# Kernel tuning notes

Hardware: AMD Instinct MI355X
Metric: run time of the kernel (lower is better)

Reference implementation:

```python
import jax, jax.numpy as jnp
import numpy as np

D_MODEL = 512
N_HEADS = 8
D_K = D_MODEL // N_HEADS


def setup_inputs() -> dict:
    key = jax.random.key(0)
    ks = jax.random.split(key, 12)
    B, L = 2, 512
    s = 1.0 / np.sqrt(D_MODEL)
    sk = 1.0 / np.sqrt(D_K)
    return {
        "query": jax.random.normal(ks[0], (B, L, D_MODEL), jnp.float32),
        "key": jax.random.normal(ks[1], (B, L, D_MODEL), jnp.float32),
        "value": jax.random.normal(ks[2], (B, L, D_MODEL), jnp.float32),
        "Wq": jax.random.normal(ks[3], (D_MODEL, D_MODEL), jnp.float32) * s,
        "bq": jnp.zeros((D_MODEL,), jnp.float32),
        "Wk": jax.random.normal(ks[4], (D_MODEL, D_MODEL), jnp.float32) * s,
        "bk": jnp.zeros((D_MODEL,), jnp.float32),
        "Wv": jax.random.normal(ks[5], (D_MODEL, D_MODEL), jnp.float32) * s,
        "bv": jnp.zeros((D_MODEL,), jnp.float32),
        "Wo": jax.random.normal(ks[6], (D_MODEL, D_MODEL), jnp.float32) * s,
        "bo": jnp.zeros((D_MODEL,), jnp.float32),
        "Aq": jax.random.normal(ks[7], (D_K, D_K), jnp.float32) * sk,  # inner W_q (no bias)
        "Ak": jax.random.normal(ks[8], (D_K, D_K), jnp.float32) * sk,  # inner W_k (no bias)
        "av": jax.random.normal(ks[9], (D_K,), jnp.float32) * sk,      # inner v (d_k -> 1)
    }


def _split_heads(x):
    B, L, _ = x.shape
    return x.reshape(B, L, N_HEADS, D_K).transpose(0, 2, 1, 3)  # [B,H,L,dk]


def reference(query, key, value, Wq, bq, Wk, bk, Wv, bv, Wo, bo, Aq, Ak, av):
    # outer projections (torch Linear: x @ W.T + b)
    Q = _split_heads(query @ Wq.T + bq)   # [B,H,Lq,dk]
    K = _split_heads(key @ Wk.T + bk)     # [B,H,Lk,dk]
    V = _split_heads(value @ Wv.T + bv)   # [B,H,Lk,dk]
    # inner additive attention: e_ij = v^T tanh(Aq q_i + Ak k_j)
    qp = Q @ Aq.T                          # [B,H,Lq,dk]
    kp = K @ Ak.T                          # [B,H,Lk,dk]
    energy = jnp.tanh(qp[:, :, :, None, :] + kp[:, :, None, :, :])  # [B,H,Lq,Lk,dk]
    scores = jnp.einsum('bhqkd,d->bhqk', energy, av)
    attn = jax.nn.softmax(scores, axis=-1)  # dropout disabled (eval)
    out = jnp.einsum('bhqk,bhkd->bhqd', attn, V)  # [B,H,Lq,dk]
    B, _, Lq, _ = out.shape
    out = out.transpose(0, 2, 1, 3).reshape(B, Lq, D_MODEL)
    return out @ Wo.T + bo
```

## Files before the change

kernel.cpp:

```cpp
#include <hip/hip_runtime.h>

#define LOG2E 1.4426950408889634f

typedef __bf16 bf16x8 __attribute__((ext_vector_type(8)));
typedef float f32x4 __attribute__((ext_vector_type(4)));
typedef float f32x2 __attribute__((ext_vector_type(2)));
typedef unsigned short u16x8 __attribute__((ext_vector_type(8)));

__device__ __forceinline__ unsigned short bfb(__bf16 b){
  union { __bf16 b; unsigned short u; } z; z.b = b; return z.u;
}


__global__ __launch_bounds__(256) void prep_all(
    const float* __restrict__ Wq, const float* __restrict__ Aq,
    const float* __restrict__ Wk, const float* __restrict__ Ak,
    const float* __restrict__ bq, const float* __restrict__ bk,
    const float* __restrict__ av,
    const float* __restrict__ Wv, const float* __restrict__ Wo,
    const float* __restrict__ Qin, const float* __restrict__ Kin,
    const float* __restrict__ Vin,
    unsigned short* __restrict__ W2qp, unsigned short* __restrict__ W2kp,
    unsigned short* __restrict__ Wvp,  unsigned short* __restrict__ Wop,
    unsigned short* __restrict__ qhi, unsigned short* __restrict__ qlo,
    unsigned short* __restrict__ khi, unsigned short* __restrict__ klo,
    unsigned short* __restrict__ vhi, unsigned short* __restrict__ vlo,
    float* __restrict__ b2q, float* __restrict__ b2k, float* __restrict__ av2g,
    float* __restrict__ zbase){
  if (blockIdx.x >= 513){
    if (blockIdx.y){
      int x = blockIdx.x - 513;
      if (x < 260){
        float* z = zbase + (size_t)(x * 256 + threadIdx.x) * 8;
        f32x4 zz = {0.f, 0.f, 0.f, 0.f};
        *(f32x4*)z = zz;
        *(f32x4*)(z + 4) = zz;
      }
      return;
    }
    int j = blockIdx.x - 513;
    const float* src; unsigned short *dh, *dl;
    if (j < 256){ src = Qin; dh = qhi; dl = qlo; }
    else if (j < 512){ src = Kin; dh = khi; dl = klo; j -= 256; }
    else { src = Vin; dh = vhi; dl = vlo; j -= 512; }
    int base = (j * 256 + threadIdx.x) * 8;
    f32x4 v0 = *(const f32x4*)(src + base);
    f32x4 v1 = *(const f32x4*)(src + base + 4);
    u16x8 hh, ll;
    #pragma unroll
    for (int t = 0; t < 8; t++){
      float f = (t < 4) ? v0[t] : v1[t - 4];
      __bf16 hb = (__bf16)f;
      hh[t] = bfb(hb);
      ll[t] = bfb((__bf16)(f - (float)hb));
    }
    *(u16x8*)(dh + base) = hh;
    *(u16x8*)(dl + base) = ll;
    return;
  }
  if (blockIdx.x >= 256){
    if (blockIdx.x == 512){
      if (blockIdx.y == 0){
        #pragma unroll
        for (int rep = 0; rep < 2; rep++){
          int n = rep * 256 + threadIdx.x;
          int h = n >> 6, e = n & 63;
          float aq = 0.f, ak = 0.f;
          for (int c = 0; c < 64; c++){
            aq += Aq[e*64 + c] * bq[h*64 + c];
            ak += Ak[e*64 + c] * bk[h*64 + c];
          }
          b2q[n] = aq * (2.f * LOG2E);
          b2k[n] = ak * (2.f * LOG2E);
        }
      } else {
        if (threadIdx.x < 64) av2g[threadIdx.x] = -2.f * LOG2E * av[threadIdx.x];
      }
      return;
    }
    const float* src = blockIdx.y ? Wo : Wv;
    unsigned short* dst = blockIdx.y ? Wop : Wvp;
    int base = ((blockIdx.x - 256) * 256 + threadIdx.x) * 4;
    int n = base >> 9, k0 = base & 511;
    float4 v = *(const float4*)(src + base);
    ushort4 h, l;
    float f; __bf16 hb;
    f = v.x; hb = (__bf16)f; h.x = bfb(hb); l.x = bfb((__bf16)(f - (float)hb));
    f = v.y; hb = (__bf16)f; h.y = bfb(hb); l.y = bfb((__bf16)(f - (float)hb));
    f = v.z; hb = (__bf16)f; h.z = bfb(hb); l.z = bfb((__bf16)(f - (float)hb));
    f = v.w; hb = (__bf16)f; h.w = bfb(hb); l.w = bfb((__bf16)(f - (float)hb));
    int nt = n >> 4, ln = n & 15;
    int ks = k0 >> 5, q = (k0 & 31) >> 3, j0 = k0 & 7;
    size_t off = (size_t)((nt*16 + ks) * 2) * 512 + (q*16 + ln) * 8 + j0;
    *(ushort4*)(dst + off)       = h;
    *(ushort4*)(dst + off + 512) = l;
    return;
  }
  const float* W  = blockIdx.y ? Wk : Wq;
  const float* Am = blockIdx.y ? Ak : Aq;
  unsigned short* dst = blockIdx.y ? W2kp : W2qp;
  int idx = blockIdx.x * 256 + threadIdx.x;
  int n = idx >> 7;
  int k0 = (idx & 127) * 4;
  int h = n >> 6, e = n & 63;
  float4 acc = {0.f, 0.f, 0.f, 0.f};
  #pragma unroll 8
  for (int c = 0; c < 64; c++){
    float am = Am[e*64 + c];
    float4 wv = *(const float4*)(W + (size_t)(h*64 + c)*512 + k0);
    acc.x += am * wv.x;
    acc.y += am * wv.y;
    acc.z += am * wv.z;
    acc.w += am * wv.w;
  }
  int nt = n >> 4, ln = n & 15;
  int ks = k0 >> 5, q = (k0 & 31) >> 3, j0 = k0 & 7;
  size_t off = (size_t)((nt*16 + ks) * 2) * 512 + (q*16 + ln) * 8 + j0;
  ushort4 hh, ll;
  float f; __bf16 hb;
  f = acc.x * (2.f * LOG2E); hb = (__bf16)f; hh.x = bfb(hb); ll.x = bfb((__bf16)(f - (float)hb));
  f = acc.y * (2.f * LOG2E); hb = (__bf16)f; hh.y = bfb(hb); ll.y = bfb((__bf16)(f - (float)hb));
  f = acc.z * (2.f * LOG2E); hb = (__bf16)f; hh.z = bfb(hb); ll.z = bfb((__bf16)(f - (float)hb));
  f = acc.w * (2.f * LOG2E); hb = (__bf16)f; hh.w = bfb(hb); ll.w = bfb((__bf16)(f - (float)hb));
  *(ushort4*)(dst + off)       = hh;
  *(ushort4*)(dst + off + 512) = ll;
}

struct GemmBatch {
  const unsigned short* Ahi;
  const unsigned short* Alo;
  const unsigned short* Bp;
  const float* bias;
  float* Cf;
  unsigned short* Chi;
  unsigned short* Clo;
  int transposed;
  int expout;
  int dual;
};
struct GemmArgs { GemmBatch g[3]; };

__global__ __launch_bounds__(256) void gemm_nk(GemmArgs ga){
  GemmBatch gb = ga.g[blockIdx.z];
  __shared__ unsigned short AhiS[64 * 40];
  __shared__ unsigned short AloS[64 * 40];
  const int tid = threadIdx.x, lane = tid & 63, w = tid >> 6;
  const int l15 = lane & 15, quad = lane >> 4;
  const int m0  = blockIdx.x * 32;
  const int nt0 = blockIdx.y * 4;
  const int wr = w >> 1, wc = w & 1;
  f32x4 ac0 = {0.f,0.f,0.f,0.f}, ac1 = ac0;

  const int srow = tid >> 3;
  const int scol = (tid & 7) * 8;
  const unsigned short* srcH = gb.Ahi + (size_t)(m0 + srow) * 512 + scol;
  const unsigned short* srcL = gb.Alo + (size_t)(m0 + srow) * 512 + scol;
  unsigned short* dstH = &AhiS[srow * 72 + scol];
  unsigned short* dstL = &AloS[srow * 72 + scol];
  u16x8 ph = *(const u16x8*)srcH;
  u16x8 pl = *(const u16x8*)srcL;

  const int arow = (wr * 16 + l15) * 72;

  for (int kc = 0; kc < 8; kc++){
    __syncthreads();
    *(u16x8*)dstH = ph;
    *(u16x8*)dstL = pl;
    if (kc < 7){
      ph = *(const u16x8*)(srcH + (kc + 1) * 64);
      pl = *(const u16x8*)(srcL + (kc + 1) * 64);
    }
    __syncthreads();
    #pragma unroll
    for (int s = 0; s < 2; s++){
      int ks = kc * 2 + s;
      bf16x8 ah = *(const bf16x8*)&AhiS[arow + s*32 + quad*8];
      bf16x8 al = *(const bf16x8*)&AloS[arow + s*32 + quad*8];
      #pragma unroll
      for (int t = 0; t < 2; t++){
        int nt = nt0 + wc*2 + t;
        const unsigned short* bp = gb.Bp + (size_t)((nt*16 + ks) * 2) * 512 + lane*8;
        bf16x8 bh = *(const bf16x8*)bp;
        bf16x8 bl = *(const bf16x8*)(bp + 512);
        f32x4& ac = t ? ac1 : ac0;
        ac = __builtin_amdgcn_mfma_f32_16x16x32_bf16(ah, bh, ac, 0, 0, 0);
        ac = __builtin_amdgcn_mfma_f32_16x16x32_bf16(al, bh, ac, 0, 0, 0);
        ac = __builtin_amdgcn_mfma_f32_16x16x32_bf16(ah, bl, ac, 0, 0, 0);
      }
    }
  }

  if (gb.dual){
    __syncthreads();
    #pragma unroll
    for (int t = 0; t < 2; t++){
      f32x4 v = t ? ac1 : ac0;
      int nl = wc*32 + t*16 + l15;
      float bs = gb.bias[nt0*16 + nl];
      #pragma unroll
      for (int r = 0; r < 4; r++){
        float val = v[r] + bs;
        int ml = wr*16 + quad*4 + r;
        __bf16 hb = (__bf16)val;
        AhiS[nl*40 + ml] = bfb(hb);
        AloS[nl*40 + ml] = bfb((__bf16)(val - (float)hb));
      }
    }
    __syncthreads();
    int nl = tid >> 2, mq = (tid & 3) * 8;
    int hh2 = (nt0 * 16) >> 6;
    int b2 = m0 >> 9;
    size_t o = (size_t)((b2*8 + hh2)*64 + ((nt0*16 + nl) & 63)) * 512 + (m0 & 511) + mq;
    *(u16x8*)(gb.Chi + o) = *(const u16x8*)&AhiS[nl*40 + mq];
    *(u16x8*)(gb.Clo + o) = *(const u16x8*)&AloS[nl*40 + mq];
    return;
  }

  const int mrow = m0 + wr * 16 + quad * 4;
  #pragma unroll
  for (int t = 0; t < 2; t++){
    f32x4 v = t ? ac1 : ac0;
    int n = nt0*16 + wc*32 + t*16 + l15;
    float bs = gb.bias[n];
    #pragma unroll
    for (int r = 0; r < 4; r++){
      float val = v[r] + bs;
      if (gb.expout) val = __builtin_amdgcn_exp2f(val);
      int m2 = mrow + r;
      if (gb.transposed){
        gb.Cf[(size_t)(((m2 >> 9) * 8 + (n >> 6)) * 512 + (m2 & 511)) * 64 + (n & 63)] = val;
      } else {
        gb.Cf[(size_t)m2 * 512 + n] = val;
      }
    }
  }
}

__global__ __launch_bounds__(512, 4) void score_pv(
    const float* __restrict__ eqQ, const float* __restrict__ ekp,
    const float* __restrict__ av2g,
    const unsigned short* __restrict__ vthi, const unsigned short* __restrict__ vtlo,
    float* __restrict__ Og, float* __restrict__ deng){
  __shared__ float SHf[12864];
  float* EKt = SHf;
  float* EQs = SHf + 8320;
  float* avS = SHf + 12800;
  unsigned short* Ph = (unsigned short*)SHf;
  unsigned short* Pl = (unsigned short*)SHf + 8704;
  float* cmb = SHf + 8704;

  const int tid = threadIdx.x, lane = tid & 63, w = tid >> 6;
  const int l15 = lane & 15, quad = lane >> 4;
  const int bh = blockIdx.z, b = bh >> 3, h = bh & 7;
  const int i0 = blockIdx.y * 64;
  const int j0 = blockIdx.x * 128;
  const int wi = w >> 1, jh = w & 1;

  if (tid < 256){
    int j = tid >> 1, c0 = (tid & 1) * 32;
    const float* s = ekp + ((size_t)(b * 512) + j0 + j) * 512 + h * 64 + c0;
    #pragma unroll
    for (int u = 0; u < 8; u++){
      f32x4 v = *(const f32x4*)(s + u * 4);
      #pragma unroll
      for (int q = 0; q < 4; q++) EKt[(c0 + u * 4 + q) * 130 + j] = v[q];
    }
  } else {
    int t2 = tid - 256;
    int r = t2 >> 2, c = (t2 & 3) * 16;
    const float* s = eqQ + ((size_t)bh * 512 + i0 + r) * 64 + c;
    #pragma unroll
    for (int u = 0; u < 4; u++)
      *(f32x4*)&EQs[r * 64 + c + u * 4] = *(const f32x4*)(s + u * 4);
    if (t2 < 64) avS[t2] = av2g[t2];
  }
  __syncthreads();

  float acc[16];
  #pragma unroll
  for (int ii = 0; ii < 16; ii++) acc[ii] = 0.f;
  const int jl = jh * 64 + lane;
  for (int d = 0; d < 64; d += 4){
    float ek0 = EKt[(d    ) * 130 + jl];
    float ek1 = EKt[(d + 1) * 130 + jl];
    float ek2 = EKt[(d + 2) * 130 + jl];
    float ek3 = EKt[(d + 3) * 130 + jl];
    f32x4 a4 = *(const f32x4*)&avS[d];
    #pragma unroll
    for (int ii = 0; ii < 16; ii++){
      f32x4 eq4 = *(const f32x4*)&EQs[(wi * 16 + ii) * 64 + d];
      float A = __builtin_fmaf(eq4[0], ek0, 1.f);
      float B = __builtin_fmaf(eq4[1], ek1, 1.f);
      float t = __builtin_fmaf(a4[1], A, a4[0] * B);
      acc[ii] = __builtin_fmaf(t, __builtin_amdgcn_rcpf(A * B), acc[ii]);
      float C = __builtin_fmaf(eq4[2], ek2, 1.f);
      float D = __builtin_fmaf(eq4[3], ek3, 1.f);
      float t2 = __builtin_fmaf(a4[3], C, a4[2] * D);
      acc[ii] = __builtin_fmaf(t2, __builtin_amdgcn_rcpf(C * D), acc[ii]);
    }
  }
  #pragma unroll
  for (int ii = 0; ii < 16; ii++) acc[ii] = __builtin_amdgcn_exp2f(acc[ii]);
  __syncthreads();

  #pragma unroll
  for (int ii = 0; ii < 16; ii++){
    float s2 = acc[ii];
    #pragma unroll
    for (int off = 1; off < 64; off <<= 1) s2 += __shfl_xor(s2, off, 64);
    if (lane == 0) atomicAdd(&deng[bh * 512 + i0 + wi * 16 + ii], s2);
    float e = acc[ii];
    __bf16 hb = (__bf16)e;
    Ph[(wi * 16 + ii) * 136 + jl] = bfb(hb);
    Pl[(wi * 16 + ii) * 136 + jl] = bfb((__bf16)(e - (float)hb));
  }

  f32x4 o0 = {0.f,0.f,0.f,0.f}, o1 = o0, o2 = o0, o3 = o0;
  const size_t vbase = ((size_t)bh * 64) * 512 + j0 + jh * 64;
  #pragma unroll
  for (int ks = 0; ks < 2; ks++){
    int k0 = jh * 64 + ks * 32 + quad * 8;
    bf16x8 pa = *(const bf16x8*)&Ph[(wi * 16 + l15) * 136 + k0];
    bf16x8 pb = *(const bf16x8*)&Pl[(wi * 16 + l15) * 136 + k0];
    #pragma unroll
    for (int nt = 0; nt < 4; nt++){
      size_t vo = vbase + (size_t)(nt * 16 + l15) * 512 + ks * 32 + quad * 8;
      bf16x8 vh = *(const bf16x8*)(vthi + vo);
      bf16x8 vl = *(const bf16x8*)(vtlo + vo);
      f32x4& o = nt == 0 ? o0 : nt == 1 ? o1 : nt == 2 ? o2 : o3;
      o = __builtin_amdgcn_mfma_f32_16x16x32_bf16(pa, vh, o, 0, 0, 0);
      o = __builtin_amdgcn_mfma_f32_16x16x32_bf16(pb, vh, o, 0, 0, 0);
      o = __builtin_amdgcn_mfma_f32_16x16x32_bf16(pa, vl, o, 0, 0, 0);
    }
  }
  if (jh == 1){
    #pragma unroll
    for (int nt = 0; nt < 4; nt++){
      f32x4 o = nt == 0 ? o0 : nt == 1 ? o1 : nt == 2 ? o2 : o3;
      #pragma unroll
      for (int r = 0; r < 4; r++)
        cmb[(wi * 16 + quad * 4 + r) * 64 + nt * 16 + l15] = o[r];
    }
  }
  __syncthreads();
  if (jh == 0){
    #pragma unroll
    for (int nt = 0; nt < 4; nt++){
      f32x4 o = nt == 0 ? o0 : nt == 1 ? o1 : nt == 2 ? o2 : o3;
      int d = nt * 16 + l15;
      #pragma unroll
      for (int r = 0; r < 4; r++){
        int il = wi * 16 + quad * 4 + r;
        float cv = o[r] + cmb[il * 64 + d];
        atomicAdd(&Og[((size_t)bh * 512 + i0 + il) * 64 + d], cv);
      }
    }
  }
}

__global__ __launch_bounds__(256) void finish_oh(
    const float* __restrict__ Og, const float* __restrict__ deng,
    unsigned short* __restrict__ Ohhi, unsigned short* __restrict__ Ohlo){
  int t = blockIdx.x * 256 + threadIdx.x;
  int bh = t >> 12;
  int i  = (t >> 3) & 511;
  int d0 = (t & 7) * 8;
  float rv = 1.0f / deng[bh * 512 + i];
  const float* src = Og + ((size_t)bh * 512 + i) * 64 + d0;
  f32x4 v0 = *(const f32x4*)src;
  f32x4 v1 = *(const f32x4*)(src + 4);
  u16x8 hh, ll;
  #pragma unroll
  for (int u = 0; u < 8; u++){
    float f = ((u < 4) ? v0[u] : v1[u - 4]) * rv;
    __bf16 hb = (__bf16)f;
    hh[u] = bfb(hb);
    ll[u] = bfb((__bf16)(f - (float)hb));
  }
  size_t o = ((size_t)(bh >> 3) * 512 + i) * 512 + (bh & 7) * 64 + d0;
  *(u16x8*)(Ohhi + o) = hh;
  *(u16x8*)(Ohlo + o) = ll;
}

extern "C" void kernel_launch(void* const* d_in, const int* in_sizes, int n_in,
                              void* d_out, int out_size, void* d_ws, size_t ws_size,
                              hipStream_t stream){
  const float* q_in = (const float*)d_in[0];
  const float* k_in = (const float*)d_in[1];
  const float* v_in = (const float*)d_in[2];
  const float* Wq_  = (const float*)d_in[3];
  const float* bq_  = (const float*)d_in[4];
  const float* Wk_  = (const float*)d_in[5];
  const float* bk_  = (const float*)d_in[6];
  const float* Wv_  = (const float*)d_in[7];
  const float* bv_  = (const float*)d_in[8];
  const float* Wo_  = (const float*)d_in[9];
  const float* bo_  = (const float*)d_in[10];
  const float* Aq_  = (const float*)d_in[11];
  const float* Ak_  = (const float*)d_in[12];
  const float* av_  = (const float*)d_in[13];

  char* ws = (char*)d_ws;
  unsigned short* W2qp = (unsigned short*)(ws + 0);
  unsigned short* W2kp = (unsigned short*)(ws + 1048576);
  unsigned short* Ohhi = (unsigned short*)(ws + 0);
  unsigned short* Ohlo = (unsigned short*)(ws + 1048576);
  unsigned short* Wvp  = (unsigned short*)(ws + 2097152);
  unsigned short* Wop  = (unsigned short*)(ws + 3145728);
  float* b2q  = (float*)(ws + 4194304);
  float* b2k  = (float*)(ws + 4196352);
  float* av2g = (float*)(ws + 4198400);
  float* eqQ  = (float*)(ws + 4198656);
  float* ekp  = (float*)(ws + 6295808);
  unsigned short* vthi = (unsigned short*)(ws + 8392960);
  unsigned short* vtlo = (unsigned short*)(ws + 9441536);
  unsigned short* qhi = (unsigned short*)(ws + 10490112);
  unsigned short* qlo = (unsigned short*)(ws + 11538688);
  unsigned short* khi = (unsigned short*)(ws + 12587264);
  unsigned short* klo = (unsigned short*)(ws + 13635840);
  unsigned short* vhi = (unsigned short*)(ws + 14684416);
  unsigned short* vlo = (unsigned short*)(ws + 15732992);
  float* deng = (float*)(ws + 16781568);
  float* Og   = (float*)(ws + 16814336);

  prep_all<<<dim3(1281, 2, 1), 256, 0, stream>>>(Wq_, Aq_, Wk_, Ak_, bq_, bk_, av_,
                                                 Wv_, Wo_, q_in, k_in, v_in,
                                                 W2qp, W2kp, Wvp, Wop,
                                                 qhi, qlo, khi, klo, vhi, vlo,
                                                 b2q, b2k, av2g, deng);

  GemmArgs ga;
  ga.g[0] = { qhi, qlo, W2qp, b2q, eqQ, 0, 0, 1, 1, 0 };
  ga.g[1] = { khi, klo, W2kp, b2k, ekp, 0, 0, 0, 1, 0 };
  ga.g[2] = { vhi, vlo, Wvp,  bv_, 0, vthi, vtlo, 0, 0, 1 };
  gemm_nk<<<dim3(32, 8, 3), 256, 0, stream>>>(ga);

  score_pv<<<dim3(4, 8, 16), 512, 0, stream>>>(eqQ, ekp, av2g, vthi, vtlo, Og, deng);

  finish_oh<<<dim3(256, 1, 1), 256, 0, stream>>>(Og, deng, Ohhi, Ohlo);

  GemmArgs go;
  go.g[0] = { Ohhi, Ohlo, Wop, bo_, (float*)d_out, 0, 0, 0, 0, 0 };
  go.g[1] = go.g[0];
  go.g[2] = go.g[0];
  gemm_nk<<<dim3(32, 8, 1), 256, 0, stream>>>(go);
}
```

Baseline: 157.4 us.

## Read Q-side operands directly from global via wave-uniform loads to shrink LDS

```diff
diff --git a/kernel.cpp b/kernel.cpp
--- a/kernel.cpp
+++ b/kernel.cpp
@@ -228,7 +228,8 @@
       if (gb.expout) val = __builtin_amdgcn_exp2f(val);
       int m2 = mrow + r;
       if (gb.transposed){
-        gb.Cf[(size_t)(((m2 >> 9) * 8 + (n >> 6)) * 512 + (m2 & 511)) * 64 + (n & 63)] = val;
+        int d = n & 63;
+        gb.Cf[(size_t)((((m2 >> 9) * 8 + (n >> 6)) * 16 + (d >> 2)) * 512 + (m2 & 511)) * 4 + (d & 3)] = val;
       } else {
         gb.Cf[(size_t)m2 * 512 + n] = val;
       }
@@ -236,18 +237,16 @@
   }
 }
 
-__global__ __launch_bounds__(512, 4) void score_pv(
+__global__ __launch_bounds__(512, 8) void score_pv(
     const float* __restrict__ eqQ, const float* __restrict__ ekp,
     const float* __restrict__ av2g,
     const unsigned short* __restrict__ vthi, const unsigned short* __restrict__ vtlo,
     float* __restrict__ Og, float* __restrict__ deng){
-  __shared__ float SHf[12864];
+  __shared__ float SHf[8704];
   float* EKt = SHf;
-  float* EQs = SHf + 8320;
-  float* avS = SHf + 12800;
   unsigned short* Ph = (unsigned short*)SHf;
   unsigned short* Pl = (unsigned short*)SHf + 8704;
-  float* cmb = SHf + 8704;
+  float* cmb = SHf;
 
   const int tid = threadIdx.x, lane = tid & 63, w = tid >> 6;
   const int l15 = lane & 15, quad = lane >> 4;
@@ -256,39 +255,35 @@
   const int j0 = blockIdx.x * 128;
   const int wi = w >> 1, jh = w & 1;
 
-  if (tid < 256){
-    int j = tid >> 1, c0 = (tid & 1) * 32;
+  {
+    int j = tid >> 2, c0 = (tid & 3) * 16;
     const float* s = ekp + ((size_t)(b * 512) + j0 + j) * 512 + h * 64 + c0;
     #pragma unroll
-    for (int u = 0; u < 8; u++){
+    for (int u = 0; u < 4; u++){
       f32x4 v = *(const f32x4*)(s + u * 4);
       #pragma unroll
       for (int q = 0; q < 4; q++) EKt[(c0 + u * 4 + q) * 130 + j] = v[q];
     }
-  } else {
-    int t2 = tid - 256;
-    int r = t2 >> 2, c = (t2 & 3) * 16;
-    const float* s = eqQ + ((size_t)bh * 512 + i0 + r) * 64 + c;
-    #pragma unroll
-    for (int u = 0; u < 4; u++)
-      *(f32x4*)&EQs[r * 64 + c + u * 4] = *(const f32x4*)(s + u * 4);
-    if (t2 < 64) avS[t2] = av2g[t2];
   }
   __syncthreads();
 
+  const int wi16 = __builtin_amdgcn_readfirstlane(wi * 16);
+  const float* eqb = eqQ + ((size_t)(bh * 16) * 512 + i0 + wi16) * 4;
+  const int jl = jh * 64 + lane;
+
   float acc[16];
   #pragma unroll
   for (int ii = 0; ii < 16; ii++) acc[ii] = 0.f;
-  const int jl = jh * 64 + lane;
-  for (int d = 0; d < 64; d += 4){
-    float ek0 = EKt[(d    ) * 130 + jl];
-    float ek1 = EKt[(d + 1) * 130 + jl];
-    float ek2 = EKt[(d + 2) * 130 + jl];
-    float ek3 = EKt[(d + 3) * 130 + jl];
-    f32x4 a4 = *(const f32x4*)&avS[d];
+  for (int ds = 0; ds < 16; ds++){
+    float ek0 = EKt[(ds * 4    ) * 130 + jl];
+    float ek1 = EKt[(ds * 4 + 1) * 130 + jl];
+    float ek2 = EKt[(ds * 4 + 2) * 130 + jl];
+    float ek3 = EKt[(ds * 4 + 3) * 130 + jl];
+    f32x4 a4 = *(const f32x4*)(av2g + ds * 4);
+    const float* ep = eqb + ds * 2048;
     #pragma unroll
     for (int ii = 0; ii < 16; ii++){
-      f32x4 eq4 = *(const f32x4*)&EQs[(wi * 16 + ii) * 64 + d];
+      f32x4 eq4 = *(const f32x4*)(ep + ii * 4);
       float A = __builtin_fmaf(eq4[0], ek0, 1.f);
       float B = __builtin_fmaf(eq4[1], ek1, 1.f);
       float t = __builtin_fmaf(a4[1], A, a4[0] * B);
@@ -308,11 +303,11 @@
     float s2 = acc[ii];
     #pragma unroll
     for (int off = 1; off < 64; off <<= 1) s2 += __shfl_xor(s2, off, 64);
-    if (lane == 0) atomicAdd(&deng[bh * 512 + i0 + wi * 16 + ii], s2);
+    if (lane == 0) atomicAdd(&deng[bh * 512 + i0 + wi16 + ii], s2);
     float e = acc[ii];
     __bf16 hb = (__bf16)e;
-    Ph[(wi * 16 + ii) * 136 + jl] = bfb(hb);
-    Pl[(wi * 16 + ii) * 136 + jl] = bfb((__bf16)(e - (float)hb));
+    Ph[(wi16 + ii) * 136 + jl] = bfb(hb);
+    Pl[(wi16 + ii) * 136 + jl] = bfb((__bf16)(e - (float)hb));
   }
 
   f32x4 o0 = {0.f,0.f,0.f,0.f}, o1 = o0, o2 = o0, o3 = o0;
@@ -320,8 +315,8 @@
   #pragma unroll
   for (int ks = 0; ks < 2; ks++){
     int k0 = jh * 64 + ks * 32 + quad * 8;
-    bf16x8 pa = *(const bf16x8*)&Ph[(wi * 16 + l15) * 136 + k0];
-    bf16x8 pb = *(const bf16x8*)&Pl[(wi * 16 + l15) * 136 + k0];
+    bf16x8 pa = *(const bf16x8*)&Ph[(wi16 + l15) * 136 + k0];
+    bf16x8 pb = *(const bf16x8*)&Pl[(wi16 + l15) * 136 + k0];
     #pragma unroll
     for (int nt = 0; nt < 4; nt++){
       size_t vo = vbase + (size_t)(nt * 16 + l15) * 512 + ks * 32 + quad * 8;
@@ -333,13 +328,14 @@
       o = __builtin_amdgcn_mfma_f32_16x16x32_bf16(pa, vl, o, 0, 0, 0);
     }
   }
+  __syncthreads();
   if (jh == 1){
     #pragma unroll
     for (int nt = 0; nt < 4; nt++){
       f32x4 o = nt == 0 ? o0 : nt == 1 ? o1 : nt == 2 ? o2 : o3;
       #pragma unroll
       for (int r = 0; r < 4; r++)
-        cmb[(wi * 16 + quad * 4 + r) * 64 + nt * 16 + l15] = o[r];
+        cmb[(wi16 + quad * 4 + r) * 64 + nt * 16 + l15] = o[r];
     }
   }
   __syncthreads();
@@ -350,7 +346,7 @@
       int d = nt * 16 + l15;
       #pragma unroll
       for (int r = 0; r < 4; r++){
-        int il = wi * 16 + quad * 4 + r;
+        int il = wi16 + quad * 4 + r;
         float cv = o[r] + cmb[il * 64 + d];
         atomicAdd(&Og[((size_t)bh * 512 + i0 + il) * 64 + d], cv);
       }
```

Measured after the change: 161.5 us. +2.6%, slower.
